# Kernel optimization log

Measured on AMD Instinct MI355X. Metric: run time of the kernel, lower is better.

## Reference

```python
import jax, jax.numpy as jnp
import numpy as np

B, N, K, C_IN, C_OUT = 4, 8192, 16, 128, 128


def setup_inputs() -> dict:
    key = jax.random.key(0)
    k1, k2, k3 = jax.random.split(key, 3)
    x = jax.random.normal(k1, (B, N, C_IN), dtype=jnp.float32)
    edge_index = jax.random.randint(k2, (2, B, N, K), 0, N, dtype=jnp.int64)
    W = jax.random.normal(k3, (C_OUT, C_IN), dtype=jnp.float32) * (1.0 / np.sqrt(C_IN))
    b = jnp.zeros((C_OUT,), dtype=jnp.float32)
    eps = jnp.zeros((1,), dtype=jnp.float32)  # eps_init = 0.0
    return {"x": x, "edge_index": edge_index, "W": W, "b": b, "eps": eps}


def reference(x, edge_index, W, b, eps):
    # x: [B, N, C], edge_index: [2, B, N, K] -- use source index edge_index[0]
    idx = edge_index[0]                                   # [B, N, K]
    # gather neighbor features per batch: x_j[b,n,k,:] = x[b, idx[b,n,k], :]
    x_j = jax.vmap(lambda xb, ib: xb[ib])(x, idx)         # [B, N, K, C]
    agg = jnp.sum(x_j, axis=2)                            # sum over neighbors -> [B, N, C]
    h = (1.0 + eps) * x + agg                             # eps-scaled residual
    # MLP([in, out], act='relu'): single linear + relu on channel dim
    out = jax.nn.relu(jnp.einsum("bnc,oc->bno", h, W) + b)
    return out
```

## Files before the change

kernel.cpp:

```cpp
#include <hip/hip_runtime.h>
#include <stdint.h>

#define BATCH   4
#define NNODE   8192
#define KNBR    16
#define CIN     128
#define COUT    128
#define MB      32
#define THREADS 256
#define HS_STRIDE 136

typedef __attribute__((ext_vector_type(8))) short short8;
typedef __attribute__((ext_vector_type(4))) float f32x4;
typedef __attribute__((ext_vector_type(4))) int   i32x4;

__device__ __forceinline__ short bf16_rne(float f) {
    union { float f; uint32_t u; } v; v.f = f;
    return (short)((v.u + 0x7FFFu + ((v.u >> 16) & 1u)) >> 16);
}
__device__ __forceinline__ float bf16_f32(short s) {
    union { uint32_t u; float f; } v; v.u = ((uint32_t)(uint16_t)s) << 16;
    return v.f;
}

__global__ __launch_bounds__(256)
void cvt_bf16(const float* __restrict__ x, ushort* __restrict__ xb) {
    const int i = blockIdx.x;
    const int j = i & 7;
    const int b = j & 3;
    const int s = i >> 3;
    const size_t base = (size_t)b * (NNODE * CIN) + (size_t)s * 2048;

    const size_t off = base + (size_t)threadIdx.x * 8;
    f32x4 a = __builtin_nontemporal_load((const f32x4*)(x + off));
    f32x4 c = __builtin_nontemporal_load((const f32x4*)(x + off) + 1);
    short8 sv;
    sv[0]=bf16_rne(a[0]); sv[1]=bf16_rne(a[1]); sv[2]=bf16_rne(a[2]); sv[3]=bf16_rne(a[3]);
    sv[4]=bf16_rne(c[0]); sv[5]=bf16_rne(c[1]); sv[6]=bf16_rne(c[2]); sv[7]=bf16_rne(c[3]);
    *(short8*)(xb + off) = sv;
}

template<bool USEBF>
__global__ __launch_bounds__(THREADS, 2)
void gin_fused(const float*  __restrict__ x,
               const ushort* __restrict__ xb,
               const int*    __restrict__ eidx,
               const float*  __restrict__ W,
               const float*  __restrict__ bias,
               const float*  __restrict__ epsp,
               float*        __restrict__ out)
{
    __shared__ __align__(16) short h_s[MB * HS_STRIDE];

    const int tid = threadIdx.x;
    const int i   = blockIdx.x;
    const int j   = i & 7;
    const int b   = j & 3;
    const int wbi = ((j >> 2) << 7) | (i >> 3);
    const int n0  = wbi * MB;
    const int row0 = b * NNODE + n0;

    const float eps1 = 1.0f + epsp[0];

    {
        const int r  = tid >> 3;
        const int q  = tid & 7;
        const int n  = n0 + r;
        const int c0 = q * 16;
        const int* ip = eidx + ((size_t)b * NNODE + n) * KNBR;

        int js[KNBR];
        #pragma unroll
        for (int p = 0; p < 4; ++p) {
            i32x4 jv = __builtin_nontemporal_load((const i32x4*)(ip + p * 4));
            js[p*4+0]=jv.x; js[p*4+1]=jv.y; js[p*4+2]=jv.z; js[p*4+3]=jv.w;
        }

        float acc[16];

        if constexpr (USEBF) {
            const ushort* xbb = xb + (size_t)b * NNODE * CIN;
            const ushort* xs  = xbb + (size_t)n * CIN + c0;
            short8 s0 = *(const short8*)xs, s1 = *(const short8*)(xs + 8);

            short8 t0[KNBR], t1[KNBR];
            #pragma unroll
            for (int k = 0; k < KNBR; ++k) {
                const ushort* xn = xbb + (size_t)js[k] * CIN + c0;
                t0[k] = *(const short8*)xn;
                t1[k] = *(const short8*)(xn + 8);
            }

            #pragma unroll
            for (int e = 0; e < 8; ++e) {
                acc[e]     = eps1 * bf16_f32(s0[e]);
                acc[8 + e] = eps1 * bf16_f32(s1[e]);
            }
            #pragma unroll
            for (int k = 0; k < KNBR; ++k) {
                #pragma unroll
                for (int e = 0; e < 8; ++e) {
                    acc[e]     += bf16_f32(t0[k][e]);
                    acc[8 + e] += bf16_f32(t1[k][e]);
                }
            }
        } else {
            const float* xbb = x + (size_t)b * NNODE * CIN;
            const float* xs  = xbb + (size_t)n * CIN + c0;
            #pragma unroll
            for (int p = 0; p < 4; ++p) {
                f32x4 v = *(const f32x4*)(xs + p * 4);
                acc[p*4+0]=eps1*v[0]; acc[p*4+1]=eps1*v[1]; acc[p*4+2]=eps1*v[2]; acc[p*4+3]=eps1*v[3];
            }
            #pragma unroll
            for (int k = 0; k < KNBR; ++k) {
                const float* xn = xbb + (size_t)js[k] * CIN + c0;
                #pragma unroll
                for (int p = 0; p < 4; ++p) {
                    f32x4 v = *(const f32x4*)(xn + p * 4);
                    acc[p*4+0]+=v[0]; acc[p*4+1]+=v[1]; acc[p*4+2]+=v[2]; acc[p*4+3]+=v[3];
                }
            }
        }

        short* hp = h_s + r * HS_STRIDE + c0;
        #pragma unroll
        for (int p = 0; p < 2; ++p) {
            short8 s;
            #pragma unroll
            for (int e = 0; e < 8; ++e) s[e] = bf16_rne(acc[p*8+e]);
            *(short8*)(hp + p * 8) = s;
        }
    }

    const int wave = tid >> 6;
    const int lane = tid & 63;
    const int l16  = lane & 15;
    const int lq   = lane >> 4;

    short8 bfrag[2][4];
    #pragma unroll
    for (int t = 0; t < 2; ++t) {
        const float* wp = W + (size_t)(wave * 32 + t * 16 + l16) * CIN;
        #pragma unroll
        for (int kb = 0; kb < 4; ++kb) {
            const float* wq = wp + kb * 32 + lq * 8;
            f32x4 f0 = *(const f32x4*)(wq);
            f32x4 f1 = *(const f32x4*)(wq + 4);
            short8 s;
            s[0]=bf16_rne(f0[0]); s[1]=bf16_rne(f0[1]); s[2]=bf16_rne(f0[2]); s[3]=bf16_rne(f0[3]);
            s[4]=bf16_rne(f1[0]); s[5]=bf16_rne(f1[1]); s[6]=bf16_rne(f1[2]); s[7]=bf16_rne(f1[3]);
            bfrag[t][kb] = s;
        }
    }
    const float bias0 = bias[wave * 32 + l16];
    const float bias1 = bias[wave * 32 + 16 + l16];

    __syncthreads();

    float* outb = out + (size_t)row0 * COUT;
    #pragma unroll
    for (int rt = 0; rt < MB / 16; ++rt) {
        const short* ap = h_s + (rt * 16 + l16) * HS_STRIDE + lq * 8;
        short8 afrag[4];
        #pragma unroll
        for (int kb = 0; kb < 4; ++kb)
            afrag[kb] = *(const short8*)(ap + kb * 32);

        #pragma unroll
        for (int t = 0; t < 2; ++t) {
            f32x4 acc = { 0.f, 0.f, 0.f, 0.f };
            #pragma unroll
            for (int kb = 0; kb < 4; ++kb)
                acc = __builtin_amdgcn_mfma_f32_16x16x32_bf16(afrag[kb], bfrag[t][kb], acc, 0, 0, 0);

            const float bv  = t ? bias1 : bias0;
            const int   col = wave * 32 + t * 16 + l16;
            #pragma unroll
            for (int ii = 0; ii < 4; ++ii) {
                const int row = rt * 16 + lq * 4 + ii;
                float v = acc[ii] + bv;
                __builtin_nontemporal_store(v > 0.f ? v : 0.f,
                                            outb + (size_t)row * COUT + col);
            }
        }
    }
}

extern "C" void kernel_launch(void* const* d_in, const int* in_sizes, int n_in,
                              void* d_out, int out_size, void* d_ws, size_t ws_size,
                              hipStream_t stream) {
    const float* x    = (const float*)d_in[0];
    const int*   eidx = (const int*)d_in[1];
    const float* W    = (const float*)d_in[2];
    const float* bias = (const float*)d_in[3];
    const float* eps  = (const float*)d_in[4];
    float*       out  = (float*)d_out;

    const size_t need = (size_t)BATCH * NNODE * CIN * sizeof(ushort);
    dim3 grid((BATCH * NNODE) / MB);

    if (ws_size >= need) {
        ushort* xb = (ushort*)d_ws;
        cvt_bf16<<<dim3(4096), dim3(256), 0, stream>>>(x, xb);
        gin_fused<true><<<grid, dim3(THREADS), 0, stream>>>(x, xb, eidx, W, bias, eps, out);
    } else {
        gin_fused<false><<<grid, dim3(THREADS), 0, stream>>>(x, nullptr, eidx, W, bias, eps, out);
    }
}
```

Before: 102.5 us.

## Schedule tiles dynamically per XCC queue and halve the conversion grid

The fused kernel now picks its tile through per-XCC atomic work queues, read from the hardware XCC_ID register, so each chiplet mostly handles one batch-half and its gathers stay in that chiplet's L2. Blocks on an XCC that drains its own queue steal from the other queues. The bf16 conversion kernel now uses linear indexing with 2048 blocks, which removes the redundant second conversion the old grid performed. In exchange it adds a memset launch, an atomic plus a block barrier at kernel start, and a fallback path that memsets the workspace even when it may be too small.

```diff
diff --git a/kernel.cpp b/kernel.cpp
--- a/kernel.cpp
+++ b/kernel.cpp
@@ -10,6 +10,9 @@
 #define THREADS 256
 #define HS_STRIDE 136
 
+#define NTILES      1024
+#define TILES_PER_Q 128
+
 typedef __attribute__((ext_vector_type(8))) short short8;
 typedef __attribute__((ext_vector_type(4))) float f32x4;
 typedef __attribute__((ext_vector_type(4))) int   i32x4;
@@ -25,13 +28,7 @@
 
 __global__ __launch_bounds__(256)
 void cvt_bf16(const float* __restrict__ x, ushort* __restrict__ xb) {
-    const int i = blockIdx.x;
-    const int j = i & 7;
-    const int b = j & 3;
-    const int s = i >> 3;
-    const size_t base = (size_t)b * (NNODE * CIN) + (size_t)s * 2048;
-
-    const size_t off = base + (size_t)threadIdx.x * 8;
+    const size_t off = ((size_t)blockIdx.x * 256 + threadIdx.x) * 8;
     f32x4 a = __builtin_nontemporal_load((const f32x4*)(x + off));
     f32x4 c = __builtin_nontemporal_load((const f32x4*)(x + off) + 1);
     short8 sv;
@@ -48,16 +45,36 @@
                const float*  __restrict__ W,
                const float*  __restrict__ bias,
                const float*  __restrict__ epsp,
-               float*        __restrict__ out)
+               float*        __restrict__ out,
+               int*          __restrict__ qctr)
 {
     __shared__ __align__(16) short h_s[MB * HS_STRIDE];
+    __shared__ int s_tile;
 
     const int tid = threadIdx.x;
-    const int i   = blockIdx.x;
-    const int j   = i & 7;
-    const int b   = j & 3;
-    const int wbi = ((j >> 2) << 7) | (i >> 3);
-    const int n0  = wbi * MB;
+
+    if (tid == 0) {
+        int xcc = 0;
+        asm volatile("s_getreg_b32 %0, hwreg(HW_REG_XCC_ID, 0, 4)" : "=s"(xcc));
+        xcc &= 7;
+        int tile = -1;
+        #pragma unroll 1
+        for (int a = 0; a < 8; ++a) {
+            const int q = (xcc + a) & 7;
+            const int t = atomicAdd(&qctr[q], 1);
+            if (t < TILES_PER_Q) {
+                tile = ((q & 3) << 8) | ((q >> 2) * TILES_PER_Q + t);
+                break;
+            }
+        }
+        s_tile = tile;
+    }
+    __syncthreads();
+
+    const int tile = s_tile;
+    const int b    = tile >> 8;
+    const int wbi  = tile & 255;
+    const int n0   = wbi * MB;
     const int row0 = b * NNODE + n0;
 
     const float eps1 = 1.0f + epsp[0];
@@ -197,14 +214,20 @@
     const float* eps  = (const float*)d_in[4];
     float*       out  = (float*)d_out;
 
-    const size_t need = (size_t)BATCH * NNODE * CIN * sizeof(ushort);
-    dim3 grid((BATCH * NNODE) / MB);
+    const size_t xb_bytes = (size_t)BATCH * NNODE * CIN * sizeof(ushort);
+    const size_t need     = xb_bytes + 64;
 
     if (ws_size >= need) {
-        ushort* xb = (ushort*)d_ws;
-        cvt_bf16<<<dim3(4096), dim3(256), 0, stream>>>(x, xb);
-        gin_fused<true><<<grid, dim3(THREADS), 0, stream>>>(x, xb, eidx, W, bias, eps, out);
+        ushort* xb   = (ushort*)d_ws;
+        int*    qctr = (int*)((char*)d_ws + xb_bytes);
+        hipMemsetAsync(qctr, 0, 64, stream);
+        cvt_bf16<<<dim3(2048), dim3(256), 0, stream>>>(x, xb);
+        gin_fused<true><<<dim3(NTILES), dim3(THREADS), 0, stream>>>(
+            x, xb, eidx, W, bias, eps, out, qctr);
     } else {
-        gin_fused<false><<<grid, dim3(THREADS), 0, stream>>>(x, nullptr, eidx, W, bias, eps, out);
-    }
-}
+        static_assert(NTILES == (BATCH * NNODE) / MB, "tile count");
+        hipMemsetAsync(d_ws, 0, ws_size < 64 ? ws_size : 64, stream);
+        gin_fused<false><<<dim3(NTILES), dim3(THREADS), 0, stream>>>(
+            x, nullptr, eidx, W, bias, eps, out, (int*)d_ws);
+    }
+}
```

After: 107.7 us. 1.05x slower.
